# Performance work log

Hardware: AMD Instinct MI355X
Metric: run time of the kernel (lower is better)

Reference implementation:

```python
import jax, jax.numpy as jnp
import numpy as np

B, N, A, O = 16, 128, 32, 64
VD, QD, H = 768, 768, 1024


def setup_inputs() -> dict:
    key = jax.random.key(0)
    ks = jax.random.split(key, 10)
    inp = {
        "q": jax.random.normal(ks[0], (B, N, 1, QD), dtype=jnp.float32),
        "att1": jax.random.uniform(ks[1], (B, N, A, O), dtype=jnp.float32),
        "obj_reps": jax.random.normal(ks[2], (B, O, VD), dtype=jnp.float32),
        "tags_attention": jax.random.randint(ks[3], (B, N, A), 0, 2, dtype=jnp.int32),
        "t": 1,
        # FCNet (weight_norm Linear + ReLU) params; dropout is identity at eval
        "vw": jax.random.normal(ks[4], (H, VD), dtype=jnp.float32) * (1.0 / np.sqrt(VD)),
        "vb": jnp.zeros((H,), dtype=jnp.float32),
        "qw": jax.random.normal(ks[5], (H, QD), dtype=jnp.float32) * (1.0 / np.sqrt(QD)),
        "qb": jnp.zeros((H,), dtype=jnp.float32),
        "lw": jax.random.normal(ks[6], (1, H), dtype=jnp.float32) * (1.0 / np.sqrt(H)),
        "lb": jnp.zeros((1,), dtype=jnp.float32),
    }
    return inp


def reference(q, att1, obj_reps, tags_attention, t, vw, vb, qw, qb, lw, lb):
    # v: [b,n,a,d] = att1 [b,n,a,o] contracted with obj_reps [b,o,d]
    v = jnp.einsum('bnao,bod->bnad', att1, obj_reps)
    # FCNet projections (weight_norm linear + ReLU, dropout off at eval)
    v_proj = jax.nn.relu(jnp.einsum('bnad,hd->bnah', v, vw) + vb)      # [b,n,a,h]
    q_proj = jax.nn.relu(jnp.einsum('bnkd,hd->bnkh', q, qw) + qb)      # [b,n,1,h]
    joint = v_proj * q_proj                                            # broadcast over a
    logits = (jnp.einsum('bnah,oh->bnao', joint, lw) + lb)[..., 0]     # [b,n,a]
    logits = logits / jnp.asarray(t, logits.dtype)
    mask = (tags_attention > 0)
    masked_logits = jnp.where(mask, logits, jnp.asarray(-1e30, logits.dtype))
    att2 = jax.nn.softmax(masked_logits, axis=-1)                       # [b,n,a]
    # att2[:,:,None,:] @ att1 -> [b,n,1,o] -> squeeze
    attention_last = jnp.einsum('bna,bnao->bno', att2, att1)
    return attention_last
```

## Files before the change

### kernel.cpp

```cpp
#include <hip/hip_runtime.h>

#define B_ 16
#define N_ 128
#define A_ 32
#define O_ 64
#define VD_ 768
#define H_ 1024

typedef short s16x8 __attribute__((ext_vector_type(8)));
typedef short s16x4 __attribute__((ext_vector_type(4)));
typedef float f32x4 __attribute__((ext_vector_type(4)));

#define MFMA(a, b, c) __builtin_amdgcn_mfma_f32_16x16x32_bf16(a, b, c, 0, 0, 0)

__device__ __forceinline__ short bf_hi(float x) {
    return (short)(__float_as_uint(x) >> 16);
}
__device__ __forceinline__ void cvthi8(const float4& f0, const float4& f1,
                                       s16x8& hi) {
    const float ff[8] = {f0.x, f0.y, f0.z, f0.w, f1.x, f1.y, f1.z, f1.w};
    #pragma unroll
    for (int e = 0; e < 8; ++e) hi[e] = bf_hi(ff[e]);
}

__device__ __forceinline__ void gload16(const void* g, void* l) {
    __builtin_amdgcn_global_load_lds(
        (const __attribute__((address_space(1))) void*)g,
        (__attribute__((address_space(3))) void*)l, 16, 0, 0);
}

__global__ __launch_bounds__(256)
void cvt_split(const float* __restrict__ obj, const float* __restrict__ q,
               const float* __restrict__ vw, const float* __restrict__ qw,
               short* __restrict__ objh, short* __restrict__ qh,
               short* __restrict__ vwh, short* __restrict__ qwh)
{
    const int bid = blockIdx.x;
    const float* src; short* hi; int base4;
    if (bid < 192)      { src = obj; hi = objh; base4 = bid * 1024; }
    else if (bid < 576) { src = q;   hi = qh;   base4 = (bid - 192) * 1024; }
    else if (bid < 768) { src = vw;  hi = vwh;  base4 = (bid - 576) * 1024; }
    else                { src = qw;  hi = qwh;  base4 = (bid - 768) * 1024; }
    #pragma unroll
    for (int it = 0; it < 4; ++it) {
        const size_t f4 = (size_t)base4 + it * 256 + threadIdx.x;
        const float4 v = *(const float4*)(src + f4 * 4);
        const float ff[4] = {v.x, v.y, v.z, v.w};
        s16x4 h4;
        #pragma unroll
        for (int e = 0; e < 4; ++e) h4[e] = bf_hi(ff[e]);
        *(s16x4*)(hi + f4 * 4) = h4;
    }
}

__global__ __launch_bounds__(256)
void gemm_split(const short* __restrict__ objh, const short* __restrict__ qh,
                const short* __restrict__ vwh, const short* __restrict__ qwh,
                const float* __restrict__ qb, const float* __restrict__ lwp,
                short* __restrict__ Wth, float* __restrict__ ub)
{
    __shared__ __align__(16) short lds2[2][2][4096];
    const int bid = blockIdx.x;
    const bool isA = bid < 256;
    const int lb_ = isA ? bid : bid - 256;
    const int r0 = (lb_ >> 4) * 64;
    const int h0 = (lb_ & 15) * 64;
    const short* Xh = isA ? objh : qh;
    const short* Bh = isA ? vwh : qwh;

    const int tid = threadIdx.x;
    const int w = tid >> 6, l = tid & 63;
    const int wm = (w >> 1) * 32, wn = (w & 1) * 32;
    const int g = l >> 4, c16 = l & 15;

    const int row0 = tid >> 3, u0 = (tid & 7) ^ (row0 & 7);
    const int unit1 = 256 + tid;
    const int row1 = unit1 >> 3, u1 = (unit1 & 7) ^ (row1 & 7);
    const short* pXh = Xh + (size_t)r0 * VD_;
    const short* pBh = Bh + (size_t)h0 * VD_;
    const int go0 = row0 * VD_ + u0 * 8;
    const int go1 = row1 * VD_ + u1 * 8;
    const int wo = w * 512;

#define STAGE(BUF, CI) do { \
        const int co_ = (CI) * 64; \
        gload16(pXh + go0 + co_, &lds2[BUF][0][wo]); \
        gload16(pXh + go1 + co_, &lds2[BUF][0][wo + 2048]); \
        gload16(pBh + go0 + co_, &lds2[BUF][1][wo]); \
        gload16(pBh + go1 + co_, &lds2[BUF][1][wo + 2048]); \
    } while (0)

    STAGE(0, 0);
    STAGE(1, 1);

    f32x4 acc[2][2] = {};

    #pragma unroll 2
    for (int c = 0; c < VD_ / 64; ++c) {
        if (c < VD_ / 64 - 1)
            asm volatile("s_waitcnt vmcnt(4)" ::: "memory");
        else
            asm volatile("s_waitcnt vmcnt(0)" ::: "memory");
        asm volatile("s_barrier" ::: "memory");

        const short* bX = &lds2[c & 1][0][0];
        const short* bB = &lds2[c & 1][1][0];
        #pragma unroll
        for (int s = 0; s < 2; ++s) {
            s16x8 ah[2], bh2[2];
            #pragma unroll
            for (int i = 0; i < 2; ++i) {
                const int m = wm + i * 16 + c16;
                const int us = (((s * 4 + g) ^ (m & 7)) * 8);
                ah[i]  = *(const s16x8*)&bX[m * 64 + us];
                const int n = wn + i * 16 + c16;
                const int vs = (((s * 4 + g) ^ (n & 7)) * 8);
                bh2[i] = *(const s16x8*)&bB[n * 64 + vs];
            }
            #pragma unroll
            for (int i = 0; i < 2; ++i)
                #pragma unroll
                for (int j = 0; j < 2; ++j)
                    acc[i][j] = MFMA(ah[i], bh2[j], acc[i][j]);
        }

        asm volatile("s_waitcnt lgkmcnt(0)" ::: "memory");
        __builtin_amdgcn_sched_barrier(0);
        asm volatile("s_barrier" ::: "memory");
        if (c + 2 < VD_ / 64) STAGE(c & 1, c + 2);
    }
#undef STAGE

    #pragma unroll
    for (int i = 0; i < 2; ++i)
        #pragma unroll
        for (int j = 0; j < 2; ++j) {
            const int h = h0 + wn + j * 16 + c16;
            if (isA) {
                const int o = wm + i * 16 + g * 4;
                s16x4 hi4;
                #pragma unroll
                for (int r = 0; r < 4; ++r) hi4[r] = bf_hi(acc[i][j][r]);
                const size_t dst = ((size_t)(lb_ >> 4) * H_ + h) * O_ + o;
                *(s16x4*)&Wth[dst] = hi4;
            } else {
                const float bv = qb[h], sv = lwp[h];
                #pragma unroll
                for (int r = 0; r < 4; ++r) {
                    const int m = r0 + wm + i * 16 + g * 4 + r;
                    ub[(size_t)m * H_ + h] = fmaxf(acc[i][j][r] + bv, 0.f) * sv;
                }
            }
        }
}

__global__ __launch_bounds__(256, 4)
void fused_logits(const float* __restrict__ att1, const short* __restrict__ Wth,
                  const float* __restrict__ ub, const float* __restrict__ vb,
                  const int* __restrict__ tags, const int* __restrict__ tptr,
                  const float* __restrict__ lbptr, float* __restrict__ out)
{
    __shared__ __align__(16) short Ah[64 * 64];
    __shared__ __align__(16) short Wc[2][4096];
    __shared__ float ut[2][1024];
    __shared__ float vbl[1024];
    __shared__ float lgp[4][64];

    const int blk = blockIdx.x;
    const int b = blk >> 6;
    const int n0 = (blk & 63) * 2;
    const int tid = threadIdx.x;
    const size_t base_row = (size_t)(b * N_ + n0) * A_;

    const int w = tid >> 6, l = tid & 63;
    const int g = l >> 4, c16 = l & 15;

    const int r0l = l >> 3;
    const int cu  = (l & 7) ^ r0l;
    const short* pW = Wth + (size_t)b * (H_ * O_) + w * 1024 + r0l * 64 + cu * 8;
    short* const dW = &Wc[0][w * 1024 + l * 8];

#define STAGEW(BUFOFF, CI) do { \
        const short* ph_ = pW + (size_t)(CI) * 4096; \
        gload16(ph_,       dW + (BUFOFF)); \
        gload16(ph_ + 512, dW + (BUFOFF) + 512); \
    } while (0)

    STAGEW(0, 0);

    {
        const int row = tid >> 2, qq = tid & 3;
        const float* src = att1 + (base_row + row) * O_ + qq * 16;
        #pragma unroll
        for (int uu = 0; uu < 2; ++uu) {
            const float4 f0 = *(const float4*)(src + uu * 8);
            const float4 f1 = *(const float4*)(src + uu * 8 + 4);
            const int us = ((qq * 2 + uu) ^ (row & 7)) * 8;
            s16x8 hi;
            cvthi8(f0, f1, hi);
            *(s16x8*)&Ah[row * 64 + us] = hi;
        }
    }

    {
        const float* u0g = ub + (size_t)(b * N_ + n0) * H_;
        const float* u1g = u0g + H_;
        *(float4*)&ut[0][tid * 4] = *(const float4*)(u0g + tid * 4);
        *(float4*)&ut[1][tid * 4] = *(const float4*)(u1g + tid * 4);
        *(float4*)&vbl[tid * 4]   = *(const float4*)(vb + tid * 4);
    }

    __syncthreads();

    s16x8 ahf[4][2];
    #pragma unroll
    for (int i = 0; i < 4; ++i)
        #pragma unroll
        for (int s = 0; s < 2; ++s) {
            const int m = i * 16 + c16;
            const int us = ((s * 4 + g) ^ (m & 7)) * 8;
            ahf[i][s] = *(const s16x8*)&Ah[m * 64 + us];
        }

    const int sr = c16 & 7;
    const int rb = w * 1024 + c16 * 64;
    const int ubo0 = (g ^ sr) * 8;
    const int ubo1 = ((g + 4) ^ sr) * 8;
    const int ulane = w * 16 + c16;

    f32x4 part[4] = {};

    #pragma unroll 2
    for (int t = 0; t < 16; ++t) {
        if (t < 15) {
            STAGEW(((t + 1) & 1) * 4096, t + 1);
            asm volatile("s_waitcnt vmcnt(2)" ::: "memory");
        } else {
            asm volatile("s_waitcnt vmcnt(0)" ::: "memory");
        }
        const int bufo = (t & 1) * 4096;
        const float vbv = vbl[t * 64 + ulane];
        const float uu0 = ut[0][t * 64 + ulane];
        const float uu1 = ut[1][t * 64 + ulane];
        const s16x8 bh0 = *(const s16x8*)&Wc[0][bufo + rb + ubo0];
        const s16x8 bh1 = *(const s16x8*)&Wc[0][bufo + rb + ubo1];
        #pragma unroll
        for (int i = 0; i < 4; ++i) {
            f32x4 acc = {};
            acc = MFMA(ahf[i][0], bh0, acc);
            acc = MFMA(ahf[i][1], bh1, acc);
            const float uu = (i < 2) ? uu0 : uu1;
            #pragma unroll
            for (int r = 0; r < 4; ++r)
                part[i][r] += fmaxf(acc[r] + vbv, 0.f) * uu;
        }
    }
#undef STAGEW

    __syncthreads();

    #pragma unroll
    for (int i = 0; i < 4; ++i)
        #pragma unroll
        for (int r = 0; r < 4; ++r) {
            float v = part[i][r];
            v += __shfl_xor(v, 1, 64);
            v += __shfl_xor(v, 2, 64);
            v += __shfl_xor(v, 4, 64);
            v += __shfl_xor(v, 8, 64);
            if (c16 == 0) lgp[w][i * 16 + g * 4 + r] = v;
        }
    __syncthreads();

    float* sml = &vbl[0];
    if (tid < 64) {
        const float tf = (float)(*tptr);
        const float lsum = lgp[0][tid] + lgp[1][tid] + lgp[2][tid] + lgp[3][tid];
        const float lv = (lsum + *lbptr) / tf;
        const int tg = tags[base_row + tid];
        sml[tid] = (tg > 0) ? lv : -1e30f;
    }
    __syncthreads();

    if (tid < 128) {
        const int nn = tid >> 6, o = tid & 63;
        const float* lr = &sml[nn * 32];
        float m = -3.0e38f;
        #pragma unroll
        for (int a = 0; a < 32; ++a) m = fmaxf(m, lr[a]);
        float s = 0.f, accum = 0.f;
        #pragma unroll
        for (int a = 0; a < 32; ++a) {
            const float e = __expf(lr[a] - m);
            s += e;
            accum += e * att1[(base_row + nn * 32 + a) * O_ + o];
        }
        out[(size_t)(b * N_ + n0 + nn) * O_ + o] = accum / s;
    }
}

extern "C" void kernel_launch(void* const* d_in, const int* in_sizes, int n_in,
                              void* d_out, int out_size, void* d_ws, size_t ws_size,
                              hipStream_t stream)
{
    const float* q    = (const float*)d_in[0];
    const float* att1 = (const float*)d_in[1];
    const float* obj  = (const float*)d_in[2];
    const int*   tags = (const int*)d_in[3];
    const int*   tptr = (const int*)d_in[4];
    const float* vw   = (const float*)d_in[5];
    const float* vb   = (const float*)d_in[6];
    const float* qw   = (const float*)d_in[7];
    const float* qb   = (const float*)d_in[8];
    const float* lw   = (const float*)d_in[9];
    const float* lb   = (const float*)d_in[10];
    float* out = (float*)d_out;

    float* ub   = (float*)d_ws;
    short* Wth  = (short*)(ub + (size_t)B_ * N_ * H_);
    short* objh = Wth + (size_t)B_ * H_ * O_;
    short* qh   = objh + (size_t)1024 * VD_;
    short* vwh  = qh + (size_t)2048 * VD_;
    short* qwh  = vwh + (size_t)H_ * VD_;

    cvt_split<<<960, 256, 0, stream>>>(obj, q, vw, qw, objh, qh, vwh, qwh);
    gemm_split<<<768, 256, 0, stream>>>(objh, qh, vwh, qwh, qb, lw, Wth, ub);
    fused_logits<<<B_ * 64, 256, 0, stream>>>(att1, Wth, ub, vb, tags,
                                              tptr, lb, out);
}
```

Measured before the change: 42.65 us.

## Triple-buffer gemm_split loads and store q-projection intermediate in bf16

The split GEMM moves from a double-buffered to a triple-buffered LDS pipeline with rotating buffer pointers, so three K-chunks are in flight and the vmcnt waits are adjusted to match. The occupancy hint is raised to three blocks. Separately, the scaled q-projection intermediate ub is written and read as bf16 instead of fp32, which halves its global write/read traffic and its LDS footprint. This costs extra LDS per block and some precision in ub, and the pointer rotation may keep the loop from unrolling.

```diff
diff --git a/kernel.cpp b/kernel.cpp
--- a/kernel.cpp
+++ b/kernel.cpp
@@ -15,6 +15,9 @@
 
 __device__ __forceinline__ short bf_hi(float x) {
     return (short)(__float_as_uint(x) >> 16);
+}
+__device__ __forceinline__ float bf2f(short s) {
+    return __uint_as_float(((unsigned)(unsigned short)s) << 16);
 }
 __device__ __forceinline__ void cvthi8(const float4& f0, const float4& f1,
                                        s16x8& hi) {
@@ -53,13 +56,13 @@
     }
 }
 
-__global__ __launch_bounds__(256)
+__global__ __launch_bounds__(256, 3)
 void gemm_split(const short* __restrict__ objh, const short* __restrict__ qh,
                 const short* __restrict__ vwh, const short* __restrict__ qwh,
                 const float* __restrict__ qb, const float* __restrict__ lwp,
-                short* __restrict__ Wth, float* __restrict__ ub)
+                short* __restrict__ Wth, short* __restrict__ ubh)
 {
-    __shared__ __align__(16) short lds2[2][2][4096];
+    __shared__ __align__(16) short lds3[3][2][4096];
     const int bid = blockIdx.x;
     const bool isA = bid < 256;
     const int lb_ = isA ? bid : bid - 256;
@@ -82,29 +85,31 @@
     const int go1 = row1 * VD_ + u1 * 8;
     const int wo = w * 512;
 
-#define STAGE(BUF, CI) do { \
+#define STAGE(BP, CI) do { \
         const int co_ = (CI) * 64; \
-        gload16(pXh + go0 + co_, &lds2[BUF][0][wo]); \
-        gload16(pXh + go1 + co_, &lds2[BUF][0][wo + 2048]); \
-        gload16(pBh + go0 + co_, &lds2[BUF][1][wo]); \
-        gload16(pBh + go1 + co_, &lds2[BUF][1][wo + 2048]); \
+        gload16(pXh + go0 + co_, (BP) + wo); \
+        gload16(pXh + go1 + co_, (BP) + wo + 2048); \
+        gload16(pBh + go0 + co_, (BP) + 4096 + wo); \
+        gload16(pBh + go1 + co_, (BP) + 4096 + wo + 2048); \
     } while (0)
 
-    STAGE(0, 0);
-    STAGE(1, 1);
+    short* b0 = &lds3[0][0][0];
+    short* b1 = &lds3[1][0][0];
+    short* b2 = &lds3[2][0][0];
+    STAGE(b0, 0);
+    STAGE(b1, 1);
+    STAGE(b2, 2);
 
     f32x4 acc[2][2] = {};
 
-    #pragma unroll 2
     for (int c = 0; c < VD_ / 64; ++c) {
-        if (c < VD_ / 64 - 1)
-            asm volatile("s_waitcnt vmcnt(4)" ::: "memory");
-        else
-            asm volatile("s_waitcnt vmcnt(0)" ::: "memory");
+        if (c < 10)      asm volatile("s_waitcnt vmcnt(8)" ::: "memory");
+        else if (c == 10) asm volatile("s_waitcnt vmcnt(4)" ::: "memory");
+        else             asm volatile("s_waitcnt vmcnt(0)" ::: "memory");
         asm volatile("s_barrier" ::: "memory");
 
-        const short* bX = &lds2[c & 1][0][0];
-        const short* bB = &lds2[c & 1][1][0];
+        const short* bX = b0;
+        const short* bB = b0 + 4096;
         #pragma unroll
         for (int s = 0; s < 2; ++s) {
             s16x8 ah[2], bh2[2];
@@ -127,7 +132,8 @@
         asm volatile("s_waitcnt lgkmcnt(0)" ::: "memory");
         __builtin_amdgcn_sched_barrier(0);
         asm volatile("s_barrier" ::: "memory");
-        if (c + 2 < VD_ / 64) STAGE(c & 1, c + 2);
+        if (c + 3 < VD_ / 64) STAGE(b0, c + 3);
+        short* tmp = b0; b0 = b1; b1 = b2; b2 = tmp;
     }
 #undef STAGE
 
@@ -148,7 +154,8 @@
                 #pragma unroll
                 for (int r = 0; r < 4; ++r) {
                     const int m = r0 + wm + i * 16 + g * 4 + r;
-                    ub[(size_t)m * H_ + h] = fmaxf(acc[i][j][r] + bv, 0.f) * sv;
+                    ubh[(size_t)m * H_ + h] =
+                        bf_hi(fmaxf(acc[i][j][r] + bv, 0.f) * sv);
                 }
             }
         }
@@ -156,13 +163,13 @@
 
 __global__ __launch_bounds__(256, 4)
 void fused_logits(const float* __restrict__ att1, const short* __restrict__ Wth,
-                  const float* __restrict__ ub, const float* __restrict__ vb,
+                  const short* __restrict__ ubh, const float* __restrict__ vb,
                   const int* __restrict__ tags, const int* __restrict__ tptr,
                   const float* __restrict__ lbptr, float* __restrict__ out)
 {
     __shared__ __align__(16) short Ah[64 * 64];
     __shared__ __align__(16) short Wc[2][4096];
-    __shared__ float ut[2][1024];
+    __shared__ short ut[2][1024];
     __shared__ float vbl[1024];
     __shared__ float lgp[4][64];
 
@@ -203,11 +210,11 @@
     }
 
     {
-        const float* u0g = ub + (size_t)(b * N_ + n0) * H_;
-        const float* u1g = u0g + H_;
-        *(float4*)&ut[0][tid * 4] = *(const float4*)(u0g + tid * 4);
-        *(float4*)&ut[1][tid * 4] = *(const float4*)(u1g + tid * 4);
-        *(float4*)&vbl[tid * 4]   = *(const float4*)(vb + tid * 4);
+        const short* u0g = ubh + (size_t)(b * N_ + n0) * H_;
+        const short* u1g = u0g + H_;
+        *(s16x4*)&ut[0][tid * 4] = *(const s16x4*)(u0g + tid * 4);
+        *(s16x4*)&ut[1][tid * 4] = *(const s16x4*)(u1g + tid * 4);
+        *(float4*)&vbl[tid * 4]  = *(const float4*)(vb + tid * 4);
     }
 
     __syncthreads();
@@ -240,8 +247,8 @@
         }
         const int bufo = (t & 1) * 4096;
         const float vbv = vbl[t * 64 + ulane];
-        const float uu0 = ut[0][t * 64 + ulane];
-        const float uu1 = ut[1][t * 64 + ulane];
+        const float uu0 = bf2f(ut[0][t * 64 + ulane]);
+        const float uu1 = bf2f(ut[1][t * 64 + ulane]);
         const s16x8 bh0 = *(const s16x8*)&Wc[0][bufo + rb + ubo0];
         const s16x8 bh1 = *(const s16x8*)&Wc[0][bufo + rb + ubo1];
         #pragma unroll
@@ -316,15 +323,15 @@
     const float* lb   = (const float*)d_in[10];
     float* out = (float*)d_out;
 
-    float* ub   = (float*)d_ws;
-    short* Wth  = (short*)(ub + (size_t)B_ * N_ * H_);
+    short* ubh  = (short*)d_ws;
+    short* Wth  = ubh + (size_t)B_ * N_ * H_;
     short* objh = Wth + (size_t)B_ * H_ * O_;
     short* qh   = objh + (size_t)1024 * VD_;
     short* vwh  = qh + (size_t)2048 * VD_;
     short* qwh  = vwh + (size_t)H_ * VD_;
 
     cvt_split<<<960, 256, 0, stream>>>(obj, q, vw, qw, objh, qh, vwh, qwh);
-    gemm_split<<<768, 256, 0, stream>>>(objh, qh, vwh, qwh, qb, lw, Wth, ub);
-    fused_logits<<<B_ * 64, 256, 0, stream>>>(att1, Wth, ub, vb, tags,
+    gemm_split<<<768, 256, 0, stream>>>(objh, qh, vwh, qwh, qb, lw, Wth, ubh);
+    fused_logits<<<B_ * 64, 256, 0, stream>>>(att1, Wth, ubh, vb, tags,
                                               tptr, lb, out);
 }
```

After: 41.31 us. 1.03x faster.
